# Performance work log

Measured on AMD Instinct MI355X. Metric: run time of the kernel, lower is better.

## Reference

```python
import jax, jax.numpy as jnp
import numpy as np

B, S, E = 1, 2048, 4096
H, D = 32, 128  # num_heads, head_dim


def setup_inputs() -> dict:
    key = jax.random.key(0)
    k1, k2, k3 = jax.random.split(key, 3)
    hidden_states = jax.random.normal(k1, (B, S, E), dtype=jnp.float32)
    # real RoPE tables (half-rotation / llama-style), base 10000
    inv_freq = 1.0 / (10000.0 ** (np.arange(0, D, 2, dtype=np.float32) / D))  # [D/2]
    pos = np.arange(S, dtype=np.float32)
    freqs = np.outer(pos, inv_freq)                      # [S, D/2]
    emb = np.concatenate([freqs, freqs], axis=-1)        # [S, D]
    cos = jnp.asarray(np.cos(emb), dtype=jnp.float32)
    sin = jnp.asarray(np.sin(emb), dtype=jnp.float32)
    w_pack = jax.random.normal(k2, (3 * E, E), dtype=jnp.float32) * (E ** -0.5)
    w_o = jax.random.normal(k3, (E, E), dtype=jnp.float32) * (E ** -0.5)
    return {"hidden_states": hidden_states, "cos": cos, "sin": sin,
            "w_pack": w_pack, "w_o": w_o}


def _rotate_half(x):
    x1, x2 = jnp.split(x, 2, axis=-1)
    return jnp.concatenate([-x2, x1], axis=-1)


def reference(hidden_states, cos, sin, w_pack, w_o):
    # fused QKV projection (W_pack, no bias)
    qkv = jnp.einsum('bse,fe->bsf', hidden_states, w_pack)      # [B,S,3E]
    q, k, v = jnp.split(qkv, 3, axis=-1)
    q = q.reshape(B, S, H, D)
    k = k.reshape(B, S, H, D)
    v = v.reshape(B, S, H, D)
    # RoPE (7B path; is_13b=False)
    c = cos[None, :, None, :]
    s = sin[None, :, None, :]
    q = q * c + _rotate_half(q) * s
    k = k * c + _rotate_half(k) * s
    # causal attention (prefill, empty past KV cache)
    scale = 1.0 / jnp.sqrt(jnp.asarray(D, dtype=q.dtype))
    scores = jnp.einsum('bqhd,bkhd->bhqk', q, k) * scale        # [B,H,S,S]
    causal = jnp.tril(jnp.ones((S, S), dtype=bool))
    scores = jnp.where(causal[None, None], scores, jnp.asarray(-1e30, scores.dtype))
    probs = jax.nn.softmax(scores, axis=-1)
    attn = jnp.einsum('bhqk,bkhd->bqhd', probs, v)              # [B,S,H,D]
    attn = attn.reshape(B, S, H * D)
    # output projection
    return jnp.einsum('bsf,ef->bse', attn, w_o)
```

## Files before the change

### kernel.cpp

```cpp
#include <hip/hip_runtime.h>

typedef unsigned short u16;
typedef unsigned int   u32;
typedef __attribute__((ext_vector_type(8))) short short8;
typedef __attribute__((ext_vector_type(4))) float f32x4;

__device__ __forceinline__ float b2f(u16 u) {
  union { float f; u32 i; } v; v.i = ((u32)u) << 16; return v.f;
}
__device__ __forceinline__ u16 f2b(float f) {
  union { float f; u32 i; } v; v.f = f;
  u32 r = v.i + 0x7fffu + ((v.i >> 16) & 1u);
  return (u16)(r >> 16);
}

__device__ __forceinline__ void gload_lds16(const void* g, void* l) {
  __builtin_amdgcn_global_load_lds(
      (const __attribute__((address_space(1))) void*)g,
      (__attribute__((address_space(3))) void*)l, 16, 0, 0);
}

template <int N> __device__ __forceinline__ void wait_vmcnt() {
  if constexpr (N == 0)      asm volatile("s_waitcnt vmcnt(0)" ::: "memory");
  else if constexpr (N == 2) asm volatile("s_waitcnt vmcnt(2)" ::: "memory");
  else if constexpr (N == 3) asm volatile("s_waitcnt vmcnt(3)" ::: "memory");
  else if constexpr (N == 4) asm volatile("s_waitcnt vmcnt(4)" ::: "memory");
  else if constexpr (N == 6) asm volatile("s_waitcnt vmcnt(6)" ::: "memory");
  else static_assert(N < 0, "unsupported vmcnt literal");
}

__device__ __forceinline__ ushort4 cvt4(float4 v) {
  ushort4 o;
  o.x = f2b(v.x); o.y = f2b(v.y); o.z = f2b(v.z); o.w = f2b(v.w);
  return o;
}

__global__ __launch_bounds__(256) void cvt_hp(const float* __restrict__ hs,
                                              const float* __restrict__ wp,
                                              u16* __restrict__ h_bf,
                                              u16* __restrict__ wp_bf) {
  const long H4 = 2097152, W4 = 12582912;
  for (long i = (long)blockIdx.x * 256 + threadIdx.x; i < H4 + W4;
       i += (long)gridDim.x * 256) {
    if (i < H4)
      ((ushort4*)h_bf)[i] = cvt4(((const float4*)hs)[i]);
    else
      ((ushort4*)wp_bf)[i - H4] = cvt4(((const float4*)wp)[i - H4]);
  }
}

__device__ __forceinline__ short8 frag_ld64(const u16* base, int rbase, int kk,
                                            int fr, int fq) {
  const int r = rbase + fr;
  return *(const short8*)(base + r * 64 + ((((kk << 2) + fq) ^ (r & 7)) << 3));
}

__global__ __launch_bounds__(512, 2) void gemm8p(const u16* __restrict__ A,
                                                 const u16* __restrict__ B,
                                                 u16* __restrict__ Cq,
                                                 u16* __restrict__ VT,
                                                 int M, int N, int K) {
  constexpr int AE = 16384;
  constexpr int BUFSZ = AE + 12288;
  __shared__ u16 lds[2 * BUFSZ];
  const int tid = threadIdx.x;
  const int wid = tid >> 6, lane = tid & 63;
  const int fr = lane & 15, fq = lane >> 4;
  const int mA = (wid >> 2) * 128;
  const int nB = (wid & 3) * 48;

  const int nty = M >> 8;
  const int qx = gridDim.x >> 3;
  const int wg = (blockIdx.x & 7) * qx + (blockIdx.x >> 3);
  const int by = wg % nty, bx = wg / nty;
  const long row0 = (long)by * 256, col0 = (long)bx * 192;

  const int rr8 = tid >> 3;
  const int jl = (tid & 7) ^ (rr8 & 7);
  const u16* gA = A + (row0 + rr8) * (long)K + jl * 8;
  const u16* gB = B + (col0 + rr8) * (long)K + jl * 8;

  f32x4 acc[8][3];
#pragma unroll
  for (int m = 0; m < 8; ++m)
#pragma unroll
    for (int n = 0; n < 3; ++n) acc[m][n] = f32x4{0.f, 0.f, 0.f, 0.f};

  const int NT = K >> 6;

  auto stageA = [&](int i, int t) {
    gload_lds16(gA + (long)(i * 64) * K + (long)t * 64,
                lds + (t & 1) * BUFSZ + (i * 512 + tid) * 8);
  };
  auto stageB = [&](int i, int t) {
    gload_lds16(gB + (long)(i * 64) * K + (long)t * 64,
                lds + (t & 1) * BUFSZ + AE + (i * 512 + tid) * 8);
  };

#pragma unroll
  for (int i = 0; i < 4; ++i) stageA(i, 0);
#pragma unroll
  for (int i = 0; i < 3; ++i) stageB(i, 0);
#pragma unroll
  for (int i = 0; i < 3; ++i) stageB(i, 1);
  wait_vmcnt<3>();
  __builtin_amdgcn_s_barrier();

  for (int t = 0; t < NT; ++t) {
    const u16* SA = lds + (t & 1) * BUFSZ;
    const u16* SB = SA + AE;
    short8 a0[4], a1[4], b0[3], b1[3];

#pragma unroll
    for (int m = 0; m < 4; ++m) a0[m] = frag_ld64(SA, mA + m * 16, 0, fr, fq);
#pragma unroll
    for (int n = 0; n < 3; ++n) b0[n] = frag_ld64(SB, nB + n * 16, 0, fr, fq);
#pragma unroll
    for (int n = 0; n < 3; ++n) b1[n] = frag_ld64(SB, nB + n * 16, 1, fr, fq);
    if (t + 1 < NT) { stageA(0, t + 1); stageA(1, t + 1); }
    __builtin_amdgcn_s_setprio(1);
#pragma unroll
    for (int m = 0; m < 4; ++m)
#pragma unroll
      for (int n = 0; n < 3; ++n)
        acc[m][n] = __builtin_amdgcn_mfma_f32_16x16x32_bf16(a0[m], b0[n], acc[m][n], 0, 0, 0);
    __builtin_amdgcn_s_setprio(0);
    asm volatile("s_waitcnt lgkmcnt(0)" ::: "memory");
    __builtin_amdgcn_s_barrier();

#pragma unroll
    for (int m = 0; m < 4; ++m) a1[m] = frag_ld64(SA, mA + 64 + m * 16, 0, fr, fq);
    if (t + 1 < NT) { stageA(2, t + 1); stageA(3, t + 1); }
    __builtin_amdgcn_s_setprio(1);
#pragma unroll
    for (int m = 0; m < 4; ++m)
#pragma unroll
      for (int n = 0; n < 3; ++n)
        acc[4 + m][n] = __builtin_amdgcn_mfma_f32_16x16x32_bf16(a1[m], b0[n], acc[4 + m][n], 0, 0, 0);
    __builtin_amdgcn_s_setprio(0);

#pragma unroll
    for (int m = 0; m < 4; ++m) a0[m] = frag_ld64(SA, mA + m * 16, 1, fr, fq);
    if (t + 2 < NT) { stageB(0, t + 2); stageB(1, t + 2); }
    __builtin_amdgcn_s_setprio(1);
#pragma unroll
    for (int m = 0; m < 4; ++m)
#pragma unroll
      for (int n = 0; n < 3; ++n)
        acc[m][n] = __builtin_amdgcn_mfma_f32_16x16x32_bf16(a0[m], b1[n], acc[m][n], 0, 0, 0);
    __builtin_amdgcn_s_setprio(0);

#pragma unroll
    for (int m = 0; m < 4; ++m) a1[m] = frag_ld64(SA, mA + 64 + m * 16, 1, fr, fq);
    if (t + 2 < NT) stageB(2, t + 2);
    __builtin_amdgcn_s_setprio(1);
#pragma unroll
    for (int m = 0; m < 4; ++m)
#pragma unroll
      for (int n = 0; n < 3; ++n)
        acc[4 + m][n] = __builtin_amdgcn_mfma_f32_16x16x32_bf16(a1[m], b1[n], acc[4 + m][n], 0, 0, 0);
    __builtin_amdgcn_s_setprio(0);
    if (t + 2 < NT) wait_vmcnt<3>();
    else            wait_vmcnt<0>();
    __builtin_amdgcn_s_barrier();
  }

#pragma unroll
  for (int m = 0; m < 8; ++m)
#pragma unroll
    for (int n = 0; n < 3; ++n) {
      const long c = col0 + nB + n * 16 + fr;
      const long rb = row0 + mA + m * 16 + fq * 4;
      if (c >= 8192) {
        ushort4 o;
        o.x = f2b(acc[m][n][0]); o.y = f2b(acc[m][n][1]);
        o.z = f2b(acc[m][n][2]); o.w = f2b(acc[m][n][3]);
        *(ushort4*)(VT + (c - 8192) * 2048 + rb) = o;
      } else {
#pragma unroll
        for (int j = 0; j < 4; ++j) Cq[(rb + j) * N + c] = f2b(acc[m][n][j]);
      }
    }
}

__global__ __launch_bounds__(256, 2) void gemm2_128(const u16* __restrict__ A,
                                                    const u16* __restrict__ B,
                                                    float* __restrict__ C,
                                                    int M, int N, int K) {
  constexpr int AE = 8192;
  constexpr int BUFSZ = 2 * AE;
  __shared__ u16 lds[2 * BUFSZ];
  const int tid = threadIdx.x;
  const int wid = tid >> 6, lane = tid & 63;
  const int fr = lane & 15, fq = lane >> 4;
  const int mA = (wid >> 1) * 64;
  const int nB = (wid & 1) * 64;

  const int nty = M >> 7;
  const int qx = gridDim.x >> 3;
  const int wg = (blockIdx.x & 7) * qx + (blockIdx.x >> 3);
  const int by = wg % nty, bx = wg / nty;
  const long row0 = (long)by * 128, col0 = (long)bx * 128;

  const int rr8 = tid >> 3;
  const int jl = (tid & 7) ^ (rr8 & 7);
  const u16* gA = A + (row0 + rr8) * (long)K + jl * 8;
  const u16* gB = B + (col0 + rr8) * (long)K + jl * 8;

  f32x4 acc[4][4];
#pragma unroll
  for (int m = 0; m < 4; ++m)
#pragma unroll
    for (int n = 0; n < 4; ++n) acc[m][n] = f32x4{0.f, 0.f, 0.f, 0.f};

  const int NT = K >> 6;

  auto stageA = [&](int i, int t) {
    gload_lds16(gA + (long)(i * 32) * K + (long)t * 64,
                lds + (t & 1) * BUFSZ + (i * 256 + tid) * 8);
  };
  auto stageB = [&](int i, int t) {
    gload_lds16(gB + (long)(i * 32) * K + (long)t * 64,
                lds + (t & 1) * BUFSZ + AE + (i * 256 + tid) * 8);
  };

#pragma unroll
  for (int i = 0; i < 4; ++i) stageA(i, 0);
#pragma unroll
  for (int i = 0; i < 4; ++i) stageB(i, 0);
#pragma unroll
  for (int i = 0; i < 4; ++i) stageB(i, 1);
  wait_vmcnt<4>();
  __builtin_amdgcn_s_barrier();

  for (int t = 0; t < NT; ++t) {
    const u16* SA = lds + (t & 1) * BUFSZ;
    const u16* SB = SA + AE;
    short8 a[2], b0[4], b1[4];

    a[0] = frag_ld64(SA, mA +  0, 0, fr, fq);
    a[1] = frag_ld64(SA, mA + 16, 0, fr, fq);
#pragma unroll
    for (int n = 0; n < 4; ++n) b0[n] = frag_ld64(SB, nB + n * 16, 0, fr, fq);
#pragma unroll
    for (int n = 0; n < 4; ++n) b1[n] = frag_ld64(SB, nB + n * 16, 1, fr, fq);
    if (t + 1 < NT) { stageA(0, t + 1); stageA(1, t + 1); }
    __builtin_amdgcn_s_setprio(1);
#pragma unroll
    for (int m = 0; m < 2; ++m)
#pragma unroll
      for (int n = 0; n < 4; ++n)
        acc[m][n] = __builtin_amdgcn_mfma_f32_16x16x32_bf16(a[m], b0[n], acc[m][n], 0, 0, 0);
    __builtin_amdgcn_s_setprio(0);
    asm volatile("s_waitcnt lgkmcnt(0)" ::: "memory");
    __builtin_amdgcn_s_barrier();

    a[0] = frag_ld64(SA, mA + 32, 0, fr, fq);
    a[1] = frag_ld64(SA, mA + 48, 0, fr, fq);
    if (t + 1 < NT) { stageA(2, t + 1); stageA(3, t + 1); }
    __builtin_amdgcn_s_setprio(1);
#pragma unroll
    for (int m = 0; m < 2; ++m)
#pragma unroll
      for (int n = 0; n < 4; ++n)
        acc[2 + m][n] = __builtin_amdgcn_mfma_f32_16x16x32_bf16(a[m], b0[n], acc[2 + m][n], 0, 0, 0);
    __builtin_amdgcn_s_setprio(0);

    a[0] = frag_ld64(SA, mA +  0, 1, fr, fq);
    a[1] = frag_ld64(SA, mA + 16, 1, fr, fq);
    if (t + 2 < NT) { stageB(0, t + 2); stageB(1, t + 2); }
    __builtin_amdgcn_s_setprio(1);
#pragma unroll
    for (int m = 0; m < 2; ++m)
#pragma unroll
      for (int n = 0; n < 4; ++n)
        acc[m][n] = __builtin_amdgcn_mfma_f32_16x16x32_bf16(a[m], b1[n], acc[m][n], 0, 0, 0);
    __builtin_amdgcn_s_setprio(0);

    a[0] = frag_ld64(SA, mA + 32, 1, fr, fq);
    a[1] = frag_ld64(SA, mA + 48, 1, fr, fq);
    if (t + 2 < NT) { stageB(2, t + 2); stageB(3, t + 2); }
    __builtin_amdgcn_s_setprio(1);
#pragma unroll
    for (int m = 0; m < 2; ++m)
#pragma unroll
      for (int n = 0; n < 4; ++n)
        acc[2 + m][n] = __builtin_amdgcn_mfma_f32_16x16x32_bf16(a[m], b1[n], acc[2 + m][n], 0, 0, 0);
    __builtin_amdgcn_s_setprio(0);
    if (t + 2 < NT) wait_vmcnt<4>();
    else            wait_vmcnt<0>();
    __builtin_amdgcn_s_barrier();
  }

#pragma unroll
  for (int m = 0; m < 4; ++m)
#pragma unroll
    for (int n = 0; n < 4; ++n)
#pragma unroll
      for (int j = 0; j < 4; ++j) {
        const long r = row0 + mA + m * 16 + fq * 4 + j;
        const long c = col0 + nB + n * 16 + fr;
        C[r * N + c] = acc[m][n][j];
      }
}

__global__ __launch_bounds__(256) void rope_wo(u16* __restrict__ qkv,
                                               const float* __restrict__ cosb,
                                               const float* __restrict__ sinb,
                                               const float* __restrict__ wo,
                                               u16* __restrict__ wo_bf) {
  if (blockIdx.x >= 8192) {
    const int n4 = 4194304;
    for (long i = (long)(blockIdx.x - 8192) * 256 + threadIdx.x; i < n4;
         i += (long)2048 * 256)
      ((ushort4*)wo_bf)[i] = cvt4(((const float4*)wo)[i]);
    return;
  }
  const int idx = blockIdx.x * 256 + threadIdx.x;
  const int dq  = idx & 15;
  const int h   = (idx >> 4) & 31;
  const int seg = (idx >> 9) & 1;
  const int s   = idx >> 10;
  const int d0  = dq * 4;
  u16* base = qkv + (long)s * 12288 + seg * 4096 + h * 128;
  const ushort4 x1 = *(const ushort4*)(base + d0);
  const ushort4 x2 = *(const ushort4*)(base + d0 + 64);
  const float4 c1 = *(const float4*)(cosb + s * 128 + d0);
  const float4 s1 = *(const float4*)(sinb + s * 128 + d0);
  const float4 c2 = *(const float4*)(cosb + s * 128 + d0 + 64);
  const float4 s2 = *(const float4*)(sinb + s * 128 + d0 + 64);
  const float scale = seg ? 1.0f : 0.08838834764831845f;
  float x1f[4] = {b2f(x1.x), b2f(x1.y), b2f(x1.z), b2f(x1.w)};
  float x2f[4] = {b2f(x2.x), b2f(x2.y), b2f(x2.z), b2f(x2.w)};
  const float c1a[4] = {c1.x, c1.y, c1.z, c1.w}, s1a[4] = {s1.x, s1.y, s1.z, s1.w};
  const float c2a[4] = {c2.x, c2.y, c2.z, c2.w}, s2a[4] = {s2.x, s2.y, s2.z, s2.w};
  ushort4 o1, o2;
  u16* o1p = (u16*)&o1; u16* o2p = (u16*)&o2;
#pragma unroll
  for (int j = 0; j < 4; ++j) {
    o1p[j] = f2b((x1f[j] * c1a[j] - x2f[j] * s1a[j]) * scale);
    o2p[j] = f2b((x2f[j] * c2a[j] + x1f[j] * s2a[j]) * scale);
  }
  *(ushort4*)(base + d0) = o1;
  *(ushort4*)(base + d0 + 64) = o2;
}

__global__ __launch_bounds__(256, 2) void attn_fwd(const u16* __restrict__ Qb,
                                                   const u16* __restrict__ Kb,
                                                   const u16* __restrict__ Vt,
                                                   u16* __restrict__ Ob) {
  const int bid = blockIdx.x;
  const int half = bid >> 8, ii = bid & 255;
  const int h = (ii >> 4) | (half << 4);
  const int qt = half ? 15 - (ii & 15) : (ii & 15);
  const int q0 = qt * 128;
  const int nt = 2 * qt + 2;
  const int tid = threadIdx.x;
  const int wid = tid >> 6, lane = tid & 63;
  const int fr = lane & 15, fq = lane >> 4;

  __shared__ u16 Ks[2][64 * 128];
  __shared__ u16 Vts[128 * 64];
  __shared__ u16 Ps[4][32 * 64];

  short8 ones;
#pragma unroll
  for (int i = 0; i < 8; ++i) ones[i] = (short)0x3F80;

  auto stageK = [&](int t, int buf) {
    const int kv0 = t * 64;
#pragma unroll
    for (int i = 0; i < 4; ++i) {
      const int c = wid * 4 + i;
      const int r = c * 4 + (lane >> 4);
      const int p = lane & 15;
      const int jsrc = p ^ (r & 7);
      gload_lds16(Kb + (long)(kv0 + r) * 12288 + h * 128 + jsrc * 8,
                  (char*)Ks[buf] + c * 1024);
    }
  };
  auto stageV = [&](int t) {
    const int kv0 = t * 64;
#pragma unroll
    for (int i = 0; i < 4; ++i) {
      const int c = wid * 4 + i;
      const int d = c * 8 + (lane >> 3);
      const int p = lane & 7;
      const int jsrc = p ^ (d & 7);
      gload_lds16(Vt + (long)(h * 128 + d) * 2048 + kv0 + jsrc * 8,
                  (char*)Vts + c * 1024);
    }
  };

  const int wq_hi = q0 + wid * 32 + 31;

  short8 qf[2][4];
#pragma unroll
  for (int m = 0; m < 2; ++m) {
    const long qrow = q0 + wid * 32 + m * 16 + fr;
#pragma unroll
    for (int kk = 0; kk < 4; ++kk)
      qf[m][kk] = *(const short8*)(Qb + qrow * 12288 + h * 128 + kk * 32 + fq * 8);
  }

  f32x4 Oacc[2][8], Sacc[2];
#pragma unroll
  for (int m = 0; m < 2; ++m) {
#pragma unroll
    for (int f = 0; f < 8; ++f) Oacc[m][f] = f32x4{0.f, 0.f, 0.f, 0.f};
    Sacc[m] = f32x4{0.f, 0.f, 0.f, 0.f};
  }
  float mrun[2];
  mrun[0] = -1e30f; mrun[1] = -1e30f;

  stageK(0, 0);
  wait_vmcnt<0>();
  __builtin_amdgcn_s_barrier();

  for (int t = 0; t < nt; ++t) {
    const int cur = t & 1;
    const int kv0 = t * 64;
    stageV(t);
    if (t + 1 < nt) stageK(t + 1, cur ^ 1);

    const bool skip = kv0 > wq_hi;
    float P[2][4][4];
    if (!skip) {
      f32x4 S[2][4];
#pragma unroll
      for (int m = 0; m < 2; ++m)
#pragma unroll
        for (int n = 0; n < 4; ++n) S[m][n] = f32x4{0.f, 0.f, 0.f, 0.f};
      __builtin_amdgcn_s_setprio(1);
#pragma unroll
      for (int kk = 0; kk < 4; ++kk) {
        short8 kf[4];
#pragma unroll
        for (int n = 0; n < 4; ++n) {
          const int r = n * 16 + fr;
          const int p = (kk * 4 + fq) ^ (r & 7);
          kf[n] = *(const short8*)((const char*)Ks[cur] + r * 256 + p * 16);
        }
#pragma unroll
        for (int m = 0; m < 2; ++m)
#pragma unroll
          for (int n = 0; n < 4; ++n)
            S[m][n] = __builtin_amdgcn_mfma_f32_16x16x32_bf16(kf[n], qf[m][kk], S[m][n], 0, 0, 0);
      }
      __builtin_amdgcn_s_setprio(0);

#pragma unroll
      for (int m = 0; m < 2; ++m) {
        const int qi = q0 + wid * 32 + m * 16 + fr;
        float tm = -1e30f;
#pragma unroll
        for (int n = 0; n < 4; ++n)
#pragma unroll
          for (int j = 0; j < 4; ++j) {
            const int kv = kv0 + n * 16 + fq * 4 + j;
            const float s = (kv <= qi) ? S[m][n][j] : -1e30f;
            P[m][n][j] = s;
            tm = fmaxf(tm, s);
          }
        tm = fmaxf(tm, __shfl_xor(tm, 16));
        tm = fmaxf(tm, __shfl_xor(tm, 32));
        if (__any(tm > mrun[m] + 8.f)) {
          const float mn = fmaxf(mrun[m], tm);
          const float al = __expf(mrun[m] - mn);
          mrun[m] = mn;
          float alr[4];
#pragma unroll
          for (int j = 0; j < 4; ++j) alr[j] = __shfl(al, fq * 4 + j);
#pragma unroll
          for (int f = 0; f < 8; ++f) {
            f32x4 o = Oacc[m][f];
#pragma unroll
            for (int j = 0; j < 4; ++j) o[j] *= alr[j];
            Oacc[m][f] = o;
          }
#pragma unroll
          for (int j = 0; j < 4; ++j) Sacc[m][j] *= alr[j];
        }
#pragma unroll
        for (int n = 0; n < 4; ++n)
#pragma unroll
          for (int j = 0; j < 4; ++j)
            P[m][n][j] = __expf(P[m][n][j] - mrun[m]);
      }

#pragma unroll
      for (int m = 0; m < 2; ++m)
#pragma unroll
        for (int n = 0; n < 4; ++n) {
          ushort4 w;
          u16* wp_ = (u16*)&w;
#pragma unroll
          for (int j = 0; j < 4; ++j) wp_[j] = f2b(P[m][n][j]);
          const int off = (m * 16 + fr) * 128 + ((n * 32 + fq * 8) ^ ((fr & 7) << 4));
          *(ushort4*)((char*)Ps[wid] + off) = w;
        }
    }

    if (t + 1 < nt) wait_vmcnt<4>();
    else            wait_vmcnt<0>();
    __builtin_amdgcn_s_barrier();

    if (!skip) {
      __builtin_amdgcn_s_setprio(1);
#pragma unroll
      for (int kb = 0; kb < 2; ++kb) {
        const int o0 = (fr) * 128 + ((kb * 64 + fq * 16) ^ ((fr & 7) << 4));
        const int o1 = (16 + fr) * 128 + ((kb * 64 + fq * 16) ^ ((fr & 7) << 4));
        short8 pa0 = *(const short8*)((const char*)Ps[wid] + o0);
        short8 pa1 = *(const short8*)((const char*)Ps[wid] + o1);
#pragma unroll
        for (int f = 0; f < 8; ++f) {
          const int d = f * 16 + fr;
          const int p = (kb * 4 + fq) ^ (d & 7);
          short8 vf = *(const short8*)((const char*)Vts + d * 128 + p * 16);
          Oacc[0][f] = __builtin_amdgcn_mfma_f32_16x16x32_bf16(pa0, vf, Oacc[0][f], 0, 0, 0);
          Oacc[1][f] = __builtin_amdgcn_mfma_f32_16x16x32_bf16(pa1, vf, Oacc[1][f], 0, 0, 0);
        }
        Sacc[0] = __builtin_amdgcn_mfma_f32_16x16x32_bf16(pa0, ones, Sacc[0], 0, 0, 0);
        Sacc[1] = __builtin_amdgcn_mfma_f32_16x16x32_bf16(pa1, ones, Sacc[1], 0, 0, 0);
      }
      __builtin_amdgcn_s_setprio(0);
    }
    wait_vmcnt<0>();
    __builtin_amdgcn_s_barrier();
  }

#pragma unroll
  for (int m = 0; m < 2; ++m)
#pragma unroll
    for (int j = 0; j < 4; ++j) {
      const float inv = 1.f / Sacc[m][j];
      const long r = q0 + wid * 32 + m * 16 + fq * 4 + j;
#pragma unroll
      for (int f = 0; f < 8; ++f)
        Ob[r * 4096 + h * 128 + f * 16 + fr] = f2b(Oacc[m][f][j] * inv);
    }
}

extern "C" void kernel_launch(void* const* d_in, const int* in_sizes, int n_in,
                              void* d_out, int out_size, void* d_ws, size_t ws_size,
                              hipStream_t stream) {
  const float* hs   = (const float*)d_in[0];
  const float* cosb = (const float*)d_in[1];
  const float* sinb = (const float*)d_in[2];
  const float* wp   = (const float*)d_in[3];
  const float* wo   = (const float*)d_in[4];
  float* out = (float*)d_out;
  char* ws = (char*)d_ws;

  u16* h_bf  = (u16*)(ws);
  u16* attn  = (u16*)(ws);
  u16* wp_bf = (u16*)(ws + 16777216);
  u16* wo_bf = (u16*)(ws + 16777216);
  u16* qkv   = (u16*)(ws + 121634816);
  u16* vt    = (u16*)(ws + 171966464);

  cvt_hp<<<4096, 256, 0, stream>>>(hs, wp, h_bf, wp_bf);
  gemm8p<<<512, 512, 0, stream>>>(h_bf, wp_bf, qkv, vt, 2048, 12288, 4096);
  rope_wo<<<10240, 256, 0, stream>>>(qkv, cosb, sinb, wo, wo_bf);
  attn_fwd<<<512, 256, 0, stream>>>(qkv, qkv + 4096, vt, attn);
  gemm2_128<<<512, 256, 0, stream>>>(attn, wo_bf, out, 2048, 4096, 4096);
}
```

Before: 419.8 us.

## Enlarge attention query tile to 256 rows per block and compute row sums in registers

The attention kernel now handles 256 query rows per block (64 per wave) instead of 128, which halves the grid to 256 blocks and doubles reuse of each staged K/V tile. The row-sum is now kept as a per-row scalar reduced with shuffles rather than computed by an extra MFMA against a ones vector. The P tile in LDS moves to a padded 72-wide layout in place of the XOR swizzle. Register use roughly doubles, so launch bounds drop to one block per SM, with 256 blocks on the device and coarser causal load balancing (largest blocks scheduled first).

```diff
diff --git a/kernel.cpp b/kernel.cpp
--- a/kernel.cpp
+++ b/kernel.cpp
@@ -345,73 +345,66 @@
   *(ushort4*)(base + d0 + 64) = o2;
 }
 
-__global__ __launch_bounds__(256, 2) void attn_fwd(const u16* __restrict__ Qb,
+__global__ __launch_bounds__(256, 1) void attn_fwd(const u16* __restrict__ Qb,
                                                    const u16* __restrict__ Kb,
                                                    const u16* __restrict__ Vt,
                                                    u16* __restrict__ Ob) {
   const int bid = blockIdx.x;
-  const int half = bid >> 8, ii = bid & 255;
-  const int h = (ii >> 4) | (half << 4);
-  const int qt = half ? 15 - (ii & 15) : (ii & 15);
-  const int q0 = qt * 128;
-  const int nt = 2 * qt + 2;
+  const int h = bid & 31;
+  const int c = 7 - (bid >> 5);
+  const int q0 = c * 256;
+  const int nt = 4 * c + 4;
   const int tid = threadIdx.x;
   const int wid = tid >> 6, lane = tid & 63;
   const int fr = lane & 15, fq = lane >> 4;
+  const int q0w = q0 + wid * 64;
 
   __shared__ u16 Ks[2][64 * 128];
   __shared__ u16 Vts[128 * 64];
-  __shared__ u16 Ps[4][32 * 64];
-
-  short8 ones;
-#pragma unroll
-  for (int i = 0; i < 8; ++i) ones[i] = (short)0x3F80;
+  __shared__ u16 Ps[4][64 * 72];
 
   auto stageK = [&](int t, int buf) {
     const int kv0 = t * 64;
 #pragma unroll
     for (int i = 0; i < 4; ++i) {
-      const int c = wid * 4 + i;
-      const int r = c * 4 + (lane >> 4);
+      const int cc = wid * 4 + i;
+      const int r = cc * 4 + (lane >> 4);
       const int p = lane & 15;
       const int jsrc = p ^ (r & 7);
       gload_lds16(Kb + (long)(kv0 + r) * 12288 + h * 128 + jsrc * 8,
-                  (char*)Ks[buf] + c * 1024);
+                  (char*)Ks[buf] + cc * 1024);
     }
   };
   auto stageV = [&](int t) {
     const int kv0 = t * 64;
 #pragma unroll
     for (int i = 0; i < 4; ++i) {
-      const int c = wid * 4 + i;
-      const int d = c * 8 + (lane >> 3);
+      const int cc = wid * 4 + i;
+      const int d = cc * 8 + (lane >> 3);
       const int p = lane & 7;
       const int jsrc = p ^ (d & 7);
       gload_lds16(Vt + (long)(h * 128 + d) * 2048 + kv0 + jsrc * 8,
-                  (char*)Vts + c * 1024);
+                  (char*)Vts + cc * 1024);
     }
   };
 
-  const int wq_hi = q0 + wid * 32 + 31;
-
-  short8 qf[2][4];
-#pragma unroll
-  for (int m = 0; m < 2; ++m) {
-    const long qrow = q0 + wid * 32 + m * 16 + fr;
+  short8 qf[4][4];
+#pragma unroll
+  for (int mm = 0; mm < 4; ++mm) {
+    const long qrow = q0w + mm * 16 + fr;
 #pragma unroll
     for (int kk = 0; kk < 4; ++kk)
-      qf[m][kk] = *(const short8*)(Qb + qrow * 12288 + h * 128 + kk * 32 + fq * 8);
-  }
-
-  f32x4 Oacc[2][8], Sacc[2];
-#pragma unroll
-  for (int m = 0; m < 2; ++m) {
-#pragma unroll
-    for (int f = 0; f < 8; ++f) Oacc[m][f] = f32x4{0.f, 0.f, 0.f, 0.f};
-    Sacc[m] = f32x4{0.f, 0.f, 0.f, 0.f};
-  }
-  float mrun[2];
-  mrun[0] = -1e30f; mrun[1] = -1e30f;
+      qf[mm][kk] = *(const short8*)(Qb + qrow * 12288 + h * 128 + kk * 32 + fq * 8);
+  }
+
+  f32x4 Oacc[4][8];
+#pragma unroll
+  for (int mm = 0; mm < 4; ++mm)
+#pragma unroll
+    for (int f = 0; f < 8; ++f) Oacc[mm][f] = f32x4{0.f, 0.f, 0.f, 0.f};
+  float mrun[4], lsum[4];
+#pragma unroll
+  for (int mm = 0; mm < 4; ++mm) { mrun[mm] = -1e30f; lsum[mm] = 0.f; }
 
   stageK(0, 0);
   wait_vmcnt<0>();
@@ -423,14 +416,13 @@
     stageV(t);
     if (t + 1 < nt) stageK(t + 1, cur ^ 1);
 
-    const bool skip = kv0 > wq_hi;
-    float P[2][4][4];
+    const bool skip = kv0 > q0w + 63;
     if (!skip) {
-      f32x4 S[2][4];
-#pragma unroll
-      for (int m = 0; m < 2; ++m)
-#pragma unroll
-        for (int n = 0; n < 4; ++n) S[m][n] = f32x4{0.f, 0.f, 0.f, 0.f};
+      f32x4 S[4][4];
+#pragma unroll
+      for (int mm = 0; mm < 4; ++mm)
+#pragma unroll
+        for (int n = 0; n < 4; ++n) S[mm][n] = f32x4{0.f, 0.f, 0.f, 0.f};
       __builtin_amdgcn_s_setprio(1);
 #pragma unroll
       for (int kk = 0; kk < 4; ++kk) {
@@ -442,63 +434,66 @@
           kf[n] = *(const short8*)((const char*)Ks[cur] + r * 256 + p * 16);
         }
 #pragma unroll
-        for (int m = 0; m < 2; ++m)
+        for (int mm = 0; mm < 4; ++mm)
 #pragma unroll
           for (int n = 0; n < 4; ++n)
-            S[m][n] = __builtin_amdgcn_mfma_f32_16x16x32_bf16(kf[n], qf[m][kk], S[m][n], 0, 0, 0);
+            S[mm][n] = __builtin_amdgcn_mfma_f32_16x16x32_bf16(kf[n], qf[mm][kk], S[mm][n], 0, 0, 0);
       }
       __builtin_amdgcn_s_setprio(0);
 
 #pragma unroll
-      for (int m = 0; m < 2; ++m) {
-        const int qi = q0 + wid * 32 + m * 16 + fr;
+      for (int mm = 0; mm < 4; ++mm) {
+        const int qi = q0w + mm * 16 + fr;
         float tm = -1e30f;
 #pragma unroll
         for (int n = 0; n < 4; ++n)
 #pragma unroll
           for (int j = 0; j < 4; ++j) {
             const int kv = kv0 + n * 16 + fq * 4 + j;
-            const float s = (kv <= qi) ? S[m][n][j] : -1e30f;
-            P[m][n][j] = s;
+            const float s = (kv <= qi) ? S[mm][n][j] : -1e30f;
+            S[mm][n][j] = s;
             tm = fmaxf(tm, s);
           }
         tm = fmaxf(tm, __shfl_xor(tm, 16));
         tm = fmaxf(tm, __shfl_xor(tm, 32));
-        if (__any(tm > mrun[m] + 8.f)) {
-          const float mn = fmaxf(mrun[m], tm);
-          const float al = __expf(mrun[m] - mn);
-          mrun[m] = mn;
+        if (__any(tm > mrun[mm] + 8.f)) {
+          const float mn = fmaxf(mrun[mm], tm);
+          const float al = __expf(mrun[mm] - mn);
+          mrun[mm] = mn;
+          lsum[mm] *= al;
           float alr[4];
 #pragma unroll
           for (int j = 0; j < 4; ++j) alr[j] = __shfl(al, fq * 4 + j);
 #pragma unroll
           for (int f = 0; f < 8; ++f) {
-            f32x4 o = Oacc[m][f];
+            f32x4 o = Oacc[mm][f];
 #pragma unroll
             for (int j = 0; j < 4; ++j) o[j] *= alr[j];
-            Oacc[m][f] = o;
+            Oacc[mm][f] = o;
           }
-#pragma unroll
-          for (int j = 0; j < 4; ++j) Sacc[m][j] *= alr[j];
         }
+        float rs = 0.f;
 #pragma unroll
         for (int n = 0; n < 4; ++n)
 #pragma unroll
-          for (int j = 0; j < 4; ++j)
-            P[m][n][j] = __expf(P[m][n][j] - mrun[m]);
-      }
-
-#pragma unroll
-      for (int m = 0; m < 2; ++m)
+          for (int j = 0; j < 4; ++j) {
+            const float p = __expf(S[mm][n][j] - mrun[mm]);
+            S[mm][n][j] = p;
+            rs += p;
+          }
+        rs += __shfl_xor(rs, 16);
+        rs += __shfl_xor(rs, 32);
+        lsum[mm] += rs;
+
 #pragma unroll
         for (int n = 0; n < 4; ++n) {
           ushort4 w;
           u16* wp_ = (u16*)&w;
 #pragma unroll
-          for (int j = 0; j < 4; ++j) wp_[j] = f2b(P[m][n][j]);
-          const int off = (m * 16 + fr) * 128 + ((n * 32 + fq * 8) ^ ((fr & 7) << 4));
-          *(ushort4*)((char*)Ps[wid] + off) = w;
+          for (int j = 0; j < 4; ++j) wp_[j] = f2b(S[mm][n][j]);
+          *(ushort4*)(Ps[wid] + (mm * 16 + fr) * 72 + n * 16 + fq * 4) = w;
         }
+      }
     }
 
     if (t + 1 < nt) wait_vmcnt<4>();
@@ -509,20 +504,19 @@
       __builtin_amdgcn_s_setprio(1);
 #pragma unroll
       for (int kb = 0; kb < 2; ++kb) {
-        const int o0 = (fr) * 128 + ((kb * 64 + fq * 16) ^ ((fr & 7) << 4));
-        const int o1 = (16 + fr) * 128 + ((kb * 64 + fq * 16) ^ ((fr & 7) << 4));
-        short8 pa0 = *(const short8*)((const char*)Ps[wid] + o0);
-        short8 pa1 = *(const short8*)((const char*)Ps[wid] + o1);
+        short8 pa[4];
+#pragma unroll
+        for (int mm = 0; mm < 4; ++mm)
+          pa[mm] = *(const short8*)(Ps[wid] + (mm * 16 + fr) * 72 + kb * 32 + fq * 8);
 #pragma unroll
         for (int f = 0; f < 8; ++f) {
           const int d = f * 16 + fr;
           const int p = (kb * 4 + fq) ^ (d & 7);
           short8 vf = *(const short8*)((const char*)Vts + d * 128 + p * 16);
-          Oacc[0][f] = __builtin_amdgcn_mfma_f32_16x16x32_bf16(pa0, vf, Oacc[0][f], 0, 0, 0);
-          Oacc[1][f] = __builtin_amdgcn_mfma_f32_16x16x32_bf16(pa1, vf, Oacc[1][f], 0, 0, 0);
+#pragma unroll
+          for (int mm = 0; mm < 4; ++mm)
+            Oacc[mm][f] = __builtin_amdgcn_mfma_f32_16x16x32_bf16(pa[mm], vf, Oacc[mm][f], 0, 0, 0);
         }
-        Sacc[0] = __builtin_amdgcn_mfma_f32_16x16x32_bf16(pa0, ones, Sacc[0], 0, 0, 0);
-        Sacc[1] = __builtin_amdgcn_mfma_f32_16x16x32_bf16(pa1, ones, Sacc[1], 0, 0, 0);
       }
       __builtin_amdgcn_s_setprio(0);
     }
@@ -531,14 +525,14 @@
   }
 
 #pragma unroll
-  for (int m = 0; m < 2; ++m)
+  for (int mm = 0; mm < 4; ++mm)
 #pragma unroll
     for (int j = 0; j < 4; ++j) {
-      const float inv = 1.f / Sacc[m][j];
-      const long r = q0 + wid * 32 + m * 16 + fq * 4 + j;
+      const float inv = 1.f / __shfl(lsum[mm], fq * 4 + j);
+      const long r = q0w + mm * 16 + fq * 4 + j;
 #pragma unroll
       for (int f = 0; f < 8; ++f)
-        Ob[r * 4096 + h * 128 + f * 16 + fr] = f2b(Oacc[m][f][j] * inv);
+        Ob[r * 4096 + h * 128 + f * 16 + fr] = f2b(Oacc[mm][f][j] * inv);
     }
 }
 
@@ -563,6 +557,6 @@
   cvt_hp<<<4096, 256, 0, stream>>>(hs, wp, h_bf, wp_bf);
   gemm8p<<<512, 512, 0, stream>>>(h_bf, wp_bf, qkv, vt, 2048, 12288, 4096);
   rope_wo<<<10240, 256, 0, stream>>>(qkv, cosb, sinb, wo, wo_bf);
-  attn_fwd<<<512, 256, 0, stream>>>(qkv, qkv + 4096, vt, attn);
+  attn_fwd<<<256, 256, 0, stream>>>(qkv, qkv + 4096, vt, attn);
   gemm2_128<<<512, 256, 0, stream>>>(attn, wo_bf, out, 2048, 4096, 4096);
 }
```

After: 461.1 us. 1.1x slower.
